# Performance work log

Measured on AMD Instinct MI355X. Metric: run time of the kernel, lower is better.

The kernel has to match this reference:

```python
import jax, jax.numpy as jnp
import numpy as np

# Synthetic production-scale triangle mesh: dense HxW grid.
H = 512
W = 512
V = H * W           # num_vertices = 262144
B = 32              # batch of meshes


def _grid_faces(h, w):
    # Two triangles per quad cell; vertex (i,j) -> index i*w + j.
    i, j = np.meshgrid(np.arange(h - 1), np.arange(w - 1), indexing='ij')
    v = (i * w + j).ravel()
    f1 = np.stack([v, v + 1, v + w], axis=1)
    f2 = np.stack([v + 1, v + w + 1, v + w], axis=1)
    return np.concatenate([f1, f2], axis=0).astype(np.int64)  # (F, 3)


def _laplacian_edges(faces, num_vertices):
    # Unique undirected edges from the 3 sides of every triangle.
    e = np.concatenate([faces[:, [0, 1]], faces[:, [1, 2]], faces[:, [2, 0]]], axis=0)
    e = np.sort(e, axis=1)
    e = np.unique(e, axis=0)                      # (E_und, 2)
    rows = np.concatenate([e[:, 0], e[:, 1]])     # directed: both orientations
    cols = np.concatenate([e[:, 1], e[:, 0]])
    deg = np.bincount(rows, minlength=num_vertices).astype(np.float32)
    vals = -1.0 / deg[rows]                       # row-normalized off-diagonal of L
    return rows.astype(np.int32), cols.astype(np.int32), vals.astype(np.float32)


def setup_inputs() -> dict:
    key = jax.random.key(0)
    faces = _grid_faces(H, W)
    rows, cols, vals = _laplacian_edges(faces, V)
    vertices = jax.random.normal(key, (B, V, 3), dtype=jnp.float32)
    return {
        'vertices': vertices,
        'rows': jnp.asarray(rows),   # (2E,) int32 — destination vertex of each Laplacian entry
        'cols': jnp.asarray(cols),   # (2E,) int32 — source   vertex of each Laplacian entry
        'vals': jnp.asarray(vals),   # (2E,) float32 — -1/deg[row]
    }


def reference(vertices, rows, cols, vals):
    # L @ v == v + scatter_add(vals * v[cols]) : identity diagonal + normalized neighbors.
    num_v = vertices.shape[1]
    gathered = vertices[:, cols, :] * vals[None, :, None]        # (B, 2E, 3)
    neigh = jax.vmap(lambda g: jax.ops.segment_sum(g, rows, num_segments=num_v))(gathered)
    Lv = vertices + neigh                                        # (B, V, 3)
    # torch: (Lv ** 2).sum(dim=-1).mean()  -> mean over (B, V) of squared norms
    return jnp.mean(jnp.sum(Lv * Lv, axis=-1))
```

## Files before the change

### kernel.cpp

```cpp
#include <hip/hip_runtime.h>


#define GH 512
#define GW 512
#define GV (GH * GW)
#define RI 16
#define NCHUNK (GH / RI)
#define ROWF (GW * 3)
#define LROW 1544
#define NITER (RI + 2)
#define NBLK (32 * NCHUNK)

__global__ __launch_bounds__(256, 4) void lap_partial_kernel(
    const float* __restrict__ verts, float* __restrict__ partials) {
    __shared__ float lds[2 * LROW];

    const int bid   = blockIdx.x;
    const int batch = bid >> 5;
    const int chunk = bid & (NCHUNK - 1);
    const int i0    = chunk * RI;
    const int t     = threadIdx.x;
    const float* __restrict__ base = verts + (size_t)batch * (GV * 3);

    if (t < 12) {
        const int slot = t / 6, o = t - 6 * slot;
        lds[slot * LROW + 1536 + o] = 0.0f;
    }

    const float jle = (t > 0)   ? 1.f : 0.f;
    const float jro = (t < 255) ? 1.f : 0.f;
    const int fL = (t == 0)   ? 1536 : (6 * t - 3);
    const int fE = 6 * t;
    const int fO = 6 * t + 3;
    const int fR = (t == 255) ? 1539 : (6 * t + 6);

    const float invE_m = -1.f / (4.f + 2.f * jle);
    const float invO_m = -1.f / (4.f + 2.f * jro);
    const float invE_t = -1.f / (2.f + 2.f * jle);
    const float invO_t = -1.f / (3.f + jro);
    const float invE_b = -1.f / (3.f + jle);
    const float invO_b = -1.f / (2.f + 2.f * jro);

    float4 a0, a1;
    {
        const int r = i0 - 1;
        if (r >= 0) {
            const float4* rp = (const float4*)(base + (size_t)r * ROWF);
            a0 = rp[t];
            a1 = (t < 128) ? rp[256 + t] : make_float4(0.f, 0.f, 0.f, 0.f);
        } else {
            a0 = make_float4(0.f, 0.f, 0.f, 0.f); a1 = a0;
        }
    }
    __syncthreads();

    float T2Ex=0,T2Ey=0,T2Ez=0, T2Ox=0,T2Oy=0,T2Oz=0;
    float T1Ex=0,T1Ey=0,T1Ez=0, T1Ox=0,T1Oy=0,T1Oz=0;
    float M1Ex=0,M1Ey=0,M1Ez=0, M1Ox=0,M1Oy=0,M1Oz=0;
    float C1Ex=0,C1Ey=0,C1Ez=0, C1Ox=0,C1Oy=0,C1Oz=0;
    float local = 0.f;

    for (int k = 0; k < NITER; ++k) {
        float* lp = lds + (k & 1) * LROW;

        *(float4*)(lp + 4 * t) = a0;
        if (t < 128) *(float4*)(lp + 1024 + 4 * t) = a1;

        if (k < NITER - 1) {
            const int rn = i0 + k;
            if (rn < GH) {
                const float4* rp = (const float4*)(base + (size_t)rn * ROWF);
                a0 = rp[t];
                a1 = (t < 128) ? rp[256 + t] : make_float4(0.f, 0.f, 0.f, 0.f);
            } else {
                a0 = make_float4(0.f, 0.f, 0.f, 0.f); a1 = a0;
            }
        }
        __syncthreads();

        const float Lx = lp[fL], Ly = lp[fL + 1], Lz = lp[fL + 2];
        const float Ex = lp[fE], Ey = lp[fE + 1], Ez = lp[fE + 2];
        const float Ox = lp[fO], Oy = lp[fO + 1], Oz = lp[fO + 2];
        const float Rx = lp[fR], Ry = lp[fR + 1], Rz = lp[fR + 2];

        const float BnEx = Ex + Lx, BnEy = Ey + Ly, BnEz = Ez + Lz;
        const float BnOx = Ox + Ex, BnOy = Oy + Ey, BnOz = Oz + Ez;
        const float TnEx = Ex + Ox, TnEy = Ey + Oy, TnEz = Ez + Oz;
        const float TnOx = Ox + Rx, TnOy = Oy + Ry, TnOz = Oz + Rz;
        const float MnEx = Lx + Ox, MnEy = Ly + Oy, MnEz = Lz + Oz;
        const float MnOx = Ex + Rx, MnOy = Ey + Ry, MnOz = Ez + Rz;

        if (k >= 2) {
            const int c = i0 + k - 2;
            float invE = invE_m, invO = invO_m;
            if (c == 0)            { invE = invE_t; invO = invO_t; }
            else if (c == GH - 1)  { invE = invE_b; invO = invO_b; }

            float s, lv;
            s = T2Ex + M1Ex + BnEx; lv = fmaf(invE, s, C1Ex); local = fmaf(lv, lv, local);
            s = T2Ey + M1Ey + BnEy; lv = fmaf(invE, s, C1Ey); local = fmaf(lv, lv, local);
            s = T2Ez + M1Ez + BnEz; lv = fmaf(invE, s, C1Ez); local = fmaf(lv, lv, local);
            s = T2Ox + M1Ox + BnOx; lv = fmaf(invO, s, C1Ox); local = fmaf(lv, lv, local);
            s = T2Oy + M1Oy + BnOy; lv = fmaf(invO, s, C1Oy); local = fmaf(lv, lv, local);
            s = T2Oz + M1Oz + BnOz; lv = fmaf(invO, s, C1Oz); local = fmaf(lv, lv, local);
        }

        T2Ex = T1Ex; T2Ey = T1Ey; T2Ez = T1Ez; T2Ox = T1Ox; T2Oy = T1Oy; T2Oz = T1Oz;
        T1Ex = TnEx; T1Ey = TnEy; T1Ez = TnEz; T1Ox = TnOx; T1Oy = TnOy; T1Oz = TnOz;
        M1Ex = MnEx; M1Ey = MnEy; M1Ez = MnEz; M1Ox = MnOx; M1Oy = MnOy; M1Oz = MnOz;
        C1Ex = Ex;   C1Ey = Ey;   C1Ez = Ez;   C1Ox = Ox;   C1Oy = Oy;   C1Oz = Oz;
    }

    #pragma unroll
    for (int off = 32; off > 0; off >>= 1)
        local += __shfl_down(local, off, 64);

    __shared__ float wsum[4];
    const int lane = t & 63;
    const int wave = t >> 6;
    if (lane == 0) wsum[wave] = local;
    __syncthreads();
    if (t == 0)
        partials[bid] = wsum[0] + wsum[1] + wsum[2] + wsum[3];
}

__global__ __launch_bounds__(256) void lap_final_kernel(
    const float* __restrict__ partials, float* __restrict__ out, int nblk, int B) {
    float local = 0.0f;
    for (int k = threadIdx.x; k < nblk; k += 256)
        local += partials[k];

    #pragma unroll
    for (int off = 32; off > 0; off >>= 1)
        local += __shfl_down(local, off, 64);

    __shared__ float wsum[4];
    const int lane = threadIdx.x & 63;
    const int wid  = threadIdx.x >> 6;
    if (lane == 0) wsum[wid] = local;
    __syncthreads();

    if (threadIdx.x == 0) {
        const float s = wsum[0] + wsum[1] + wsum[2] + wsum[3];
        out[0] = s / ((float)B * (float)GV);
    }
}

extern "C" void kernel_launch(void* const* d_in, const int* in_sizes, int n_in,
                              void* d_out, int out_size, void* d_ws, size_t ws_size,
                              hipStream_t stream) {
    const float* verts = (const float*)d_in[0];
    float* out = (float*)d_out;
    float* partials = (float*)d_ws;

    const int B = in_sizes[0] / (GV * 3);

    lap_partial_kernel<<<NBLK, 256, 0, stream>>>(verts, partials);
    lap_final_kernel<<<1, 256, 0, stream>>>(partials, out, NBLK, B);
}
```

Measured before the change: 159.3 us.

## Replace LDS row staging with direct per-thread loads and wave shuffles

Removes the double-buffered LDS tile and per-row __syncthreads. Each thread now loads its own two vertices straight from global memory, gets its left and right neighbours through wave shuffles, and wave-edge lanes fetch halo values directly. Rows per block drop from 16 to 8, doubling the grid, and the occupancy hint rises to 6. The goal is to cut barrier and LDS overhead and gain parallelism. In exchange, global loads are 12-byte strided per thread instead of coalesced float4, the redundant halo-row reads grow with the smaller chunks, and edge lanes add divergent scalar loads.

```diff
diff --git a/kernel.cpp b/kernel.cpp
--- a/kernel.cpp
+++ b/kernel.cpp
@@ -4,36 +4,24 @@
 #define GH 512
 #define GW 512
 #define GV (GH * GW)
-#define RI 16
+#define ROWF (GW * 3)
+#define RI 8
 #define NCHUNK (GH / RI)
-#define ROWF (GW * 3)
-#define LROW 1544
 #define NITER (RI + 2)
 #define NBLK (32 * NCHUNK)
 
-__global__ __launch_bounds__(256, 4) void lap_partial_kernel(
+__global__ __launch_bounds__(256, 6) void lap_partial_kernel(
     const float* __restrict__ verts, float* __restrict__ partials) {
-    __shared__ float lds[2 * LROW];
-
     const int bid   = blockIdx.x;
-    const int batch = bid >> 5;
+    const int batch = bid >> 6;
     const int chunk = bid & (NCHUNK - 1);
     const int i0    = chunk * RI;
-    const int t     = threadIdx.x;
-    const float* __restrict__ base = verts + (size_t)batch * (GV * 3);
+    const int p     = threadIdx.x;
+    const int lane  = p & 63;
+    const float* __restrict__ pcol = verts + (size_t)batch * (GV * 3) + 6 * p;
 
-    if (t < 12) {
-        const int slot = t / 6, o = t - 6 * slot;
-        lds[slot * LROW + 1536 + o] = 0.0f;
-    }
-
-    const float jle = (t > 0)   ? 1.f : 0.f;
-    const float jro = (t < 255) ? 1.f : 0.f;
-    const int fL = (t == 0)   ? 1536 : (6 * t - 3);
-    const int fE = 6 * t;
-    const int fO = 6 * t + 3;
-    const int fR = (t == 255) ? 1539 : (6 * t + 6);
-
+    const float jle = (p > 0)   ? 1.f : 0.f;
+    const float jro = (p < 255) ? 1.f : 0.f;
     const float invE_m = -1.f / (4.f + 2.f * jle);
     const float invO_m = -1.f / (4.f + 2.f * jro);
     const float invE_t = -1.f / (2.f + 2.f * jle);
@@ -41,47 +29,34 @@
     const float invE_b = -1.f / (3.f + jle);
     const float invO_b = -1.f / (2.f + 2.f * jro);
 
-    float4 a0, a1;
-    {
-        const int r = i0 - 1;
-        if (r >= 0) {
-            const float4* rp = (const float4*)(base + (size_t)r * ROWF);
-            a0 = rp[t];
-            a1 = (t < 128) ? rp[256 + t] : make_float4(0.f, 0.f, 0.f, 0.f);
-        } else {
-            a0 = make_float4(0.f, 0.f, 0.f, 0.f); a1 = a0;
-        }
-    }
-    __syncthreads();
-
     float T2Ex=0,T2Ey=0,T2Ez=0, T2Ox=0,T2Oy=0,T2Oz=0;
     float T1Ex=0,T1Ey=0,T1Ez=0, T1Ox=0,T1Oy=0,T1Oz=0;
     float M1Ex=0,M1Ey=0,M1Ez=0, M1Ox=0,M1Oy=0,M1Oz=0;
     float C1Ex=0,C1Ey=0,C1Ez=0, C1Ox=0,C1Oy=0,C1Oz=0;
     float local = 0.f;
 
+    #pragma unroll 2
     for (int k = 0; k < NITER; ++k) {
-        float* lp = lds + (k & 1) * LROW;
+        const int r = i0 - 1 + k;
 
-        *(float4*)(lp + 4 * t) = a0;
-        if (t < 128) *(float4*)(lp + 1024 + 4 * t) = a1;
-
-        if (k < NITER - 1) {
-            const int rn = i0 + k;
-            if (rn < GH) {
-                const float4* rp = (const float4*)(base + (size_t)rn * ROWF);
-                a0 = rp[t];
-                a1 = (t < 128) ? rp[256 + t] : make_float4(0.f, 0.f, 0.f, 0.f);
-            } else {
-                a0 = make_float4(0.f, 0.f, 0.f, 0.f); a1 = a0;
+        float Ex=0,Ey=0,Ez=0, Ox=0,Oy=0,Oz=0;
+        float hlx=0,hly=0,hlz=0, hrx=0,hry=0,hrz=0;
+        if (r >= 0 && r < GH) {
+            const float* __restrict__ rp = pcol + (size_t)r * ROWF;
+            Ex = rp[0]; Ey = rp[1]; Ez = rp[2];
+            Ox = rp[3]; Oy = rp[4]; Oz = rp[5];
+            if (lane == 0 && p > 0) {
+                hlx = rp[-3]; hly = rp[-2]; hlz = rp[-1];
+            }
+            if (lane == 63 && p < 255) {
+                hrx = rp[6]; hry = rp[7]; hrz = rp[8];
             }
         }
-        __syncthreads();
 
-        const float Lx = lp[fL], Ly = lp[fL + 1], Lz = lp[fL + 2];
-        const float Ex = lp[fE], Ey = lp[fE + 1], Ez = lp[fE + 2];
-        const float Ox = lp[fO], Oy = lp[fO + 1], Oz = lp[fO + 2];
-        const float Rx = lp[fR], Ry = lp[fR + 1], Rz = lp[fR + 2];
+        float Lx = __shfl_up(Ox, 1, 64), Ly = __shfl_up(Oy, 1, 64), Lz = __shfl_up(Oz, 1, 64);
+        float Rx = __shfl_down(Ex, 1, 64), Ry = __shfl_down(Ey, 1, 64), Rz = __shfl_down(Ez, 1, 64);
+        if (lane == 0)  { Lx = hlx; Ly = hly; Lz = hlz; }
+        if (lane == 63) { Rx = hrx; Ry = hry; Rz = hrz; }
 
         const float BnEx = Ex + Lx, BnEy = Ey + Ly, BnEz = Ez + Lz;
         const float BnOx = Ox + Ex, BnOy = Oy + Ey, BnOz = Oz + Ez;
@@ -93,8 +68,8 @@
         if (k >= 2) {
             const int c = i0 + k - 2;
             float invE = invE_m, invO = invO_m;
-            if (c == 0)            { invE = invE_t; invO = invO_t; }
-            else if (c == GH - 1)  { invE = invE_b; invO = invO_b; }
+            if (c == 0)           { invE = invE_t; invO = invO_t; }
+            else if (c == GH - 1) { invE = invE_b; invO = invO_b; }
 
             float s, lv;
             s = T2Ex + M1Ex + BnEx; lv = fmaf(invE, s, C1Ex); local = fmaf(lv, lv, local);
@@ -116,11 +91,10 @@
         local += __shfl_down(local, off, 64);
 
     __shared__ float wsum[4];
-    const int lane = t & 63;
-    const int wave = t >> 6;
+    const int wave = p >> 6;
     if (lane == 0) wsum[wave] = local;
     __syncthreads();
-    if (t == 0)
+    if (p == 0)
         partials[bid] = wsum[0] + wsum[1] + wsum[2] + wsum[3];
 }
 
```

New measurement: 165.2 us. 1.04x slower.
